# Kernel tuning notes

Measured on AMD Instinct MI355X. Metric: run time of the kernel, lower is better.

## Reference

```python
import jax, jax.numpy as jnp
import numpy as np

EMBED_DIM = 512

def setup_inputs() -> dict:
    key = jax.random.key(0)
    ks = jax.random.split(key, 5)
    D = EMBED_DIM
    x = jax.random.normal(ks[0], (4, 2048, D), dtype=jnp.float32)
    # qkv projection: weight [3D, D] (torch layout), bias [3D]
    qkv_w = jax.random.normal(ks[1], (3 * D, D), dtype=jnp.float32) * (D ** -0.5)
    qkv_b = jax.random.normal(ks[2], (3 * D,), dtype=jnp.float32) * 0.02
    out_w = jax.random.normal(ks[3], (D, D), dtype=jnp.float32) * (D ** -0.5)
    out_b = jax.random.normal(ks[4], (D,), dtype=jnp.float32) * 0.02
    return {"x": x, "qkv_w": qkv_w, "qkv_b": qkv_b, "out_w": out_w, "out_b": out_b}

def reference(x, qkv_w, qkv_b, out_w, out_b):
    D = x.shape[-1]
    scaling = D ** -0.5
    # qkv: [B, S, 3D]
    qkv = jnp.einsum('bsd,ed->bse', x, qkv_w) + qkv_b
    q, k, v = jnp.split(qkv, 3, axis=-1)
    q = q * scaling
    # scores: [B, S, S]
    attn = jnp.einsum('bqd,bkd->bqk', q, k)
    attn = jax.nn.softmax(attn, axis=-1)
    # dropout p=0.0 -> identity (eval-mode equivalent)
    out = jnp.einsum('bqk,bkd->bqd', attn, v)
    out = jnp.einsum('bsd,ed->bse', out, out_w) + out_b
    return out
```

## Files before the change

kernel.cpp:

```cpp
#include <hip/hip_runtime.h>

typedef _Float16 f16;
typedef _Float16 f16x2 __attribute__((ext_vector_type(2)));
typedef _Float16 f16x4 __attribute__((ext_vector_type(4)));
typedef _Float16 f16x8 __attribute__((ext_vector_type(8)));
typedef float f32x4 __attribute__((ext_vector_type(4)));
typedef float f32x16 __attribute__((ext_vector_type(16)));

#define MFMA16(a, b, c) __builtin_amdgcn_mfma_f32_16x16x32_f16((a), (b), (c), 0, 0, 0)
#define MFMA32(a, b, c) __builtin_amdgcn_mfma_f32_32x32x16_f16((a), (b), (c), 0, 0, 0)

typedef const __attribute__((address_space(1))) void gv_t;
typedef __attribute__((address_space(3))) void lv_t;

__global__ void cvt_all(const float* __restrict__ x, const float* __restrict__ qw,
                        const float* __restrict__ ow, f16* __restrict__ d) {
    int i = (blockIdx.x * 256 + threadIdx.x) * 4;
    const float* s;
    int off;
    if (i < 4194304) { s = x; off = i; }
    else if (i < 4980736) { s = qw; off = i - 4194304; }
    else { s = ow; off = i - 4980736; }
    float4 v = *(const float4*)(s + off);
    f16x4 o = {(f16)v.x, (f16)v.y, (f16)v.z, (f16)v.w};
    *(f16x4*)(d + i) = o;
}

template<int MODE>
__global__ __launch_bounds__(256, 3) void gemm_nt(const f16* __restrict__ A, const f16* __restrict__ W,
                                                  const float* __restrict__ bias, float* __restrict__ Cf,
                                                  f16* __restrict__ Qb, f16* __restrict__ Kb,
                                                  f16* __restrict__ Vt) {
    __shared__ f16 As[2][128 * 32];
    __shared__ f16 Bs[2][128 * 32];
    const int m0 = blockIdx.x * 128, n0 = blockIdx.y * 128;
    const int tid = threadIdx.x;
    const int w = tid >> 6, l = tid & 63;
    const int wm = w >> 1, wn = w & 1;
    const int lr = l & 15, lg = l >> 4;
    const int R = w * 16 + (l >> 2);
    const int ldsoff = w * 512;
    const int lidx = ldsoff + l * 8;
    const f16* ag = A + (size_t)(m0 + R) * 512 + (l & 3) * 8;
    const f16* bg = W + (size_t)(n0 + R) * 512 + (l & 3) * 8;
    (void)lidx;

#if __has_builtin(__builtin_amdgcn_global_load_lds)
#define GLDS(gp, lp) __builtin_amdgcn_global_load_lds((gv_t*)(gp), (lv_t*)(lp), 16, 0, 0)
#define STAGE(k0, buf) do {                                   \
        GLDS(ag + (k0), &As[buf][ldsoff]);                    \
        GLDS(ag + 64 * 512 + (k0), &As[buf][ldsoff + 2048]);  \
        GLDS(bg + (k0), &Bs[buf][ldsoff]);                    \
        GLDS(bg + 64 * 512 + (k0), &Bs[buf][ldsoff + 2048]);  \
    } while (0)
#else
#define STAGE(k0, buf) do {                                                      \
        *(f16x8*)&As[buf][lidx] = *(const f16x8*)(ag + (k0));                    \
        *(f16x8*)&As[buf][lidx + 2048] = *(const f16x8*)(ag + 64 * 512 + (k0));  \
        *(f16x8*)&Bs[buf][lidx] = *(const f16x8*)(bg + (k0));                    \
        *(f16x8*)&Bs[buf][lidx + 2048] = *(const f16x8*)(bg + 64 * 512 + (k0));  \
    } while (0)
#endif

    f32x4 acc[4][4] = {};
    STAGE(0, 0);
    __syncthreads();
    int cur = 0;
    for (int k0 = 0; k0 < 512; k0 += 32) {
        if (k0 + 32 < 512) STAGE(k0 + 32, cur ^ 1);
        f16x8 af[4], bf[4];
#pragma unroll
        for (int i = 0; i < 4; ++i) af[i] = *(f16x8*)&As[cur][(64 * wm + 16 * i + lr) * 32 + lg * 8];
#pragma unroll
        for (int i = 0; i < 4; ++i) bf[i] = *(f16x8*)&Bs[cur][(64 * wn + 16 * i + lr) * 32 + lg * 8];
        __builtin_amdgcn_s_setprio(1);
#pragma unroll
        for (int mf = 0; mf < 4; ++mf)
#pragma unroll
            for (int nf = 0; nf < 4; ++nf) acc[mf][nf] = MFMA16(af[mf], bf[nf], acc[mf][nf]);
        __builtin_amdgcn_s_setprio(0);
        __syncthreads();
        cur ^= 1;
    }
#pragma unroll
    for (int mf = 0; mf < 4; ++mf)
#pragma unroll
        for (int nf = 0; nf < 4; ++nf)
#pragma unroll
            for (int r = 0; r < 4; ++r) {
                int rr = 64 * wm + 16 * mf + 4 * lg + r;
                int cc = 64 * wn + 16 * nf + lr;
                int m = m0 + rr, e = n0 + cc;
                float val = acc[mf][nf][r] + bias[e];
                if (MODE == 0) {
                    int bb = m >> 11, s = m & 2047;
                    if (e < 512) {
                        Qb[((size_t)bb * 2048 + s) * 512 + e] = (f16)(val * 0.04419417382415922f);
                    } else if (e < 1024) {
                        int d = e - 512;
                        Kb[((((size_t)bb * 64 + (s >> 5)) * 32 + (d >> 4)) * 64
                            + ((d >> 3) & 1) * 32 + (s & 31)) * 8 + (d & 7)] = (f16)val;
                    } else {
                        int d = e - 1024;
                        Vt[((((size_t)bb * 16 + (d >> 5)) * 128 + (s >> 4)) * 64
                            + ((s >> 3) & 1) * 32 + (d & 31)) * 8 + (s & 7)] = (f16)val;
                    }
                } else {
                    Cf[(size_t)m * 512 + e] = val;
                }
            }
#undef STAGE
}

template<int NSPLIT, bool PART>
__global__ __launch_bounds__(512, 2) void flash_attn(const f16* __restrict__ Qb, const f16* __restrict__ Kb,
                                                     const f16* __restrict__ Vt, f16* __restrict__ AO,
                                                     f16* __restrict__ Opart, float* __restrict__ Ml) {
    __shared__ f16 Qs[32 * 512];
    __shared__ f16 P_lds[32 * 256];
    __shared__ float mbuf[32][8];
    __shared__ float lbuf[32][8];
    __shared__ float abuf[32];

    const int bid = blockIdx.x;
    const int xcd = bid & 7, slot = bid >> 3;
    const int b = xcd >> 1;
    const int t = slot * 2 + (xcd & 1);
    const int q0 = (t / NSPLIT) * 32;
    const int ks = t % NSPLIT;
    const int SPLITLEN = 2048 / NSPLIT;
    const int nkt = SPLITLEN / 256;

    const int tid = threadIdx.x;
    const int j = tid >> 6, l = tid & 63;
    const int q = l & 31, lh = l >> 5;

    const f16* Qg = Qb + ((size_t)b * 2048 + q0) * 512;
    const f16* Kg = Kb + ((size_t)b * 64 + (size_t)ks * (SPLITLEN / 32)) * 32 * 512;
    const f16* Vg = Vt + (size_t)b * 16 * 128 * 512 + (size_t)(ks * (SPLITLEN / 16)) * 512;

    for (int i = tid; i < 2048; i += 512) {
        int r = i >> 6, ch = i & 63;
        *(f16x8*)&Qs[r * 512 + ((ch ^ (r & 7)) * 8)] = *(const f16x8*)&Qg[(size_t)r * 512 + ch * 8];
    }

    f32x16 o[2] = {};
    float m_st = -1e30f, l_st = 0.f;
    char* Pq = (char*)&P_lds[0];
    const uint swz = ((uint)(q & 15)) << 4;
    const int qbase = q * 512, qx = q & 7;
    f16x8 kr[16], vr[8];
    {
        const f16* kp0 = Kg + (size_t)j * 32 * 512 + (size_t)l * 8;
#pragma unroll
        for (int i = 0; i < 16; ++i) kr[i] = *(const f16x8*)(kp0 + (size_t)i * 512);
    }
    __syncthreads();

    for (int kt = 0; kt < nkt; ++kt) {
        const int key0 = kt * 256;
        const f16* kp = Kg + ((size_t)((key0 >> 5) + j) * 32) * 512 + (size_t)l * 8;
        const f16* vpb = Vg + ((size_t)(2 * j) * 128 + (key0 >> 4)) * 512 + (size_t)l * 8;
#pragma unroll
        for (int i = 0; i < 4; ++i) {
            vr[2 * i] = *(const f16x8*)(vpb + (size_t)i * 512);
            vr[2 * i + 1] = *(const f16x8*)(vpb + (size_t)(128 + i) * 512);
        }
        f32x16 sA = {}, sB = {};
        __builtin_amdgcn_s_setprio(1);
#pragma unroll
        for (int kc = 0; kc < 32; kc += 2) {
            f16x8 k0 = kr[kc & 15];
            f16x8 k1 = kr[(kc & 15) + 1];
            if (kc < 16) {
                kr[kc] = *(const f16x8*)(kp + (size_t)(kc + 16) * 512);
                kr[kc + 1] = *(const f16x8*)(kp + (size_t)(kc + 17) * 512);
            }
            f16x8 q0f = *(f16x8*)&Qs[qbase + (((2 * kc + lh) ^ qx) * 8)];
            f16x8 q1f = *(f16x8*)&Qs[qbase + (((2 * kc + 2 + lh) ^ qx) * 8)];
            sA = MFMA32(k0, q0f, sA);
            sB = MFMA32(k1, q1f, sB);
        }
        __builtin_amdgcn_s_setprio(0);
        float s[16];
#pragma unroll
        for (int r = 0; r < 16; ++r) s[r] = sA[r] + sB[r];
        float mt = s[0];
#pragma unroll
        for (int r = 1; r < 16; ++r) mt = fmaxf(mt, s[r]);
        mt = fmaxf(mt, __shfl_xor(mt, 32));
        if (l < 32) mbuf[q][j] = mt;
        __syncthreads();
        float mnew = m_st;
        {
            float4 mv0 = *(float4*)&mbuf[q][0];
            float4 mv1 = *(float4*)&mbuf[q][4];
            mnew = fmaxf(mnew, fmaxf(fmaxf(mv0.x, mv0.y), fmaxf(mv0.z, mv0.w)));
            mnew = fmaxf(mnew, fmaxf(fmaxf(mv1.x, mv1.y), fmaxf(mv1.z, mv1.w)));
        }
        float alpha = __expf(m_st - mnew);
        if (l < 32) abuf[q] = alpha;
        float ps = 0.f;
#pragma unroll
        for (int r = 0; r < 16; ++r) {
            s[r] = __expf(s[r] - mnew);
            ps += s[r];
        }
        ps += __shfl_xor(ps, 32);
        if (l < 32) lbuf[q][j] = ps;
        {
            const uint rowb = (uint)q * 512;
#pragma unroll
            for (int i = 0; i < 4; ++i) {
                int key = 8 * i + 4 * lh + 32 * j;
                f16x4 pk = {(f16)s[4 * i], (f16)s[4 * i + 1], (f16)s[4 * i + 2], (f16)s[4 * i + 3]};
                *(f16x4*)(Pq + ((rowb + (uint)key * 2) ^ swz)) = pk;
            }
        }
        m_st = mnew;
        __syncthreads();
        if (kt + 1 < nkt) {
            const f16* kpn = Kg + ((size_t)(((key0 + 256) >> 5) + j) * 32) * 512 + (size_t)l * 8;
#pragma unroll
            for (int i = 0; i < 16; ++i) kr[i] = *(const f16x8*)(kpn + (size_t)i * 512);
        }
        {
            float4 lv0 = *(float4*)&lbuf[q][0];
            float4 lv1 = *(float4*)&lbuf[q][4];
            l_st = l_st * alpha + ((lv0.x + lv0.y) + (lv0.z + lv0.w))
                                + ((lv1.x + lv1.y) + (lv1.z + lv1.w));
        }
        float av[4][4];
#pragma unroll
        for (int g = 0; g < 4; ++g) {
            float4 a4 = *(float4*)&abuf[8 * g + 4 * lh];
            av[g][0] = a4.x; av[g][1] = a4.y; av[g][2] = a4.z; av[g][3] = a4.w;
        }
#pragma unroll
        for (int dt = 0; dt < 2; ++dt)
#pragma unroll
            for (int r = 0; r < 16; ++r) o[dt][r] *= av[r >> 2][r & 3];
        __builtin_amdgcn_s_setprio(1);
#pragma unroll
        for (int kk = 0; kk < 16; ++kk) {
            f16x8 v0 = vr[(kk & 3) * 2];
            f16x8 v1 = vr[(kk & 3) * 2 + 1];
            if (kk < 12) {
                vr[(kk & 3) * 2] = *(const f16x8*)(vpb + (size_t)(kk + 4) * 512);
                vr[(kk & 3) * 2 + 1] = *(const f16x8*)(vpb + (size_t)(128 + kk + 4) * 512);
            }
            f16x8 paf = *(f16x8*)(Pq + (((uint)q * 512 + (uint)(16 * kk + 8 * lh) * 2) ^ swz));
            o[0] = MFMA32(paf, v0, o[0]);
            o[1] = MFMA32(paf, v1, o[1]);
        }
        __builtin_amdgcn_s_setprio(0);
    }
    __syncthreads();
    if (l < 32) abuf[q] = l_st;
    if (PART && l < 32 && j == 0) {
        Ml[((size_t)bid * 32 + q) * 2 + 0] = m_st;
        Ml[((size_t)bid * 32 + q) * 2 + 1] = l_st;
    }
    __syncthreads();
    float iv[4][4];
#pragma unroll
    for (int g = 0; g < 4; ++g) {
        float4 a4 = *(float4*)&abuf[8 * g + 4 * lh];
        iv[g][0] = 1.f / a4.x; iv[g][1] = 1.f / a4.y; iv[g][2] = 1.f / a4.z; iv[g][3] = 1.f / a4.w;
    }
    f16* op = PART ? (Opart + (size_t)bid * 32 * 512 + 64 * j)
                   : (AO + ((size_t)(b * 2048 + q0)) * 512 + 64 * j);
#pragma unroll
    for (int r = 0; r < 16; ++r) {
        int qr = (r & 3) + 8 * (r >> 2) + 4 * lh;
        float inv = iv[r >> 2][r & 3];
#pragma unroll
        for (int dt = 0; dt < 2; ++dt)
            op[(size_t)qr * 512 + 32 * dt + q] = (f16)(o[dt][r] * inv);
    }
}

template<int NS>
__global__ __launch_bounds__(256) void combineN(const f16* __restrict__ Opart, const float* __restrict__ Ml,
                                                f16* __restrict__ AO) {
    int gid = blockIdx.x * 256 + threadIdx.x;
    int row = gid >> 6, col0 = (gid & 63) * 8;
    int b = row >> 11, qq = row & 2047;
    int qb = qq >> 5, qr = qq & 31;
    int bids[NS];
    float m[NS], ll[NS];
#pragma unroll
    for (int s = 0; s < NS; ++s) {
        int t = qb * NS + s;
        bids[s] = (t >> 1) * 8 + 2 * b + (t & 1);
        m[s] = Ml[((size_t)bids[s] * 32 + qr) * 2];
        ll[s] = Ml[((size_t)bids[s] * 32 + qr) * 2 + 1];
    }
    float M = m[0];
#pragma unroll
    for (int s = 1; s < NS; ++s) M = fmaxf(M, m[s]);
    float c[NS], W = 0.f;
#pragma unroll
    for (int s = 0; s < NS; ++s) {
        c[s] = __expf(m[s] - M) * ll[s];
        W += c[s];
    }
    float invW = 1.f / W;
    float av[8] = {};
#pragma unroll
    for (int s = 0; s < NS; ++s) {
        f16x8 v = *(const f16x8*)&Opart[((size_t)bids[s] * 32 + qr) * 512 + col0];
        float cs = c[s] * invW;
#pragma unroll
        for (int jj = 0; jj < 8; ++jj) av[jj] += cs * (float)v[jj];
    }
    f16x8 o8;
#pragma unroll
    for (int jj = 0; jj < 8; ++jj) o8[jj] = (f16)av[jj];
    *(f16x8*)&AO[(size_t)row * 512 + col0] = o8;
}

extern "C" void kernel_launch(void* const* d_in, const int* in_sizes, int n_in,
                              void* d_out, int out_size, void* d_ws, size_t ws_size,
                              hipStream_t stream) {
    (void)in_sizes; (void)n_in; (void)out_size;
    const float* x = (const float*)d_in[0];
    const float* qkv_w = (const float*)d_in[1];
    const float* qkv_b = (const float*)d_in[2];
    const float* out_w = (const float*)d_in[3];
    const float* out_b = (const float*)d_in[4];
    char* ws = (char*)d_ws;
    f16* xh    = (f16*)(ws + 0);
    f16* wqkvh = (f16*)(ws + 8388608);
    f16* wouth = (f16*)(ws + 9961472);
    f16* Qb    = (f16*)(ws + 10485760);
    f16* Kb    = (f16*)(ws + 18874368);
    f16* Vt    = (f16*)(ws + 27262976);
    f16* AO    = (f16*)(ws + 35651584);
    f16* Opart = (f16*)(ws + 44040192);
    float* Ml  = (float*)(ws + 44040192 + 16777216);
    const size_t NEED = 44040192ull + 16777216ull + 131072ull;
    (void)wqkvh; (void)wouth;

    cvt_all<<<5120, 256, 0, stream>>>(x, qkv_w, out_w, xh);

    gemm_nt<0><<<dim3(64, 12), 256, 0, stream>>>(xh, wqkvh, qkv_b, nullptr, Qb, Kb, Vt);

    if (ws_size >= NEED) {
        flash_attn<2, true><<<512, 512, 0, stream>>>(Qb, Kb, Vt, nullptr, Opart, Ml);
        combineN<2><<<2048, 256, 0, stream>>>(Opart, Ml, AO);
    } else {
        flash_attn<1, false><<<256, 512, 0, stream>>>(Qb, Kb, Vt, AO, nullptr, nullptr);
    }

    gemm_nt<1><<<dim3(64, 4), 256, 0, stream>>>(AO, wouth, out_b, (float*)d_out,
                                                nullptr, nullptr, nullptr);
}
```

Measured before the change: 118.0 us.

## Process 64 query rows per flash-attention block to reuse K/V tiles

Each attention block now handles 64 query rows instead of 32, so every K and V fragment loaded from global memory feeds two MFMAs, one per 32-row half. The grid is halved and the combine kernel and partial buffer indexing are updated for 64-row blocks. This is meant to halve K/V global traffic per query, at the cost of doubled LDS usage, more accumulator registers, and only 256 blocks, which may leave compute units underused.

```diff
diff --git a/kernel.cpp b/kernel.cpp
--- a/kernel.cpp
+++ b/kernel.cpp
@@ -116,17 +116,17 @@
 __global__ __launch_bounds__(512, 2) void flash_attn(const f16* __restrict__ Qb, const f16* __restrict__ Kb,
                                                      const f16* __restrict__ Vt, f16* __restrict__ AO,
                                                      f16* __restrict__ Opart, float* __restrict__ Ml) {
-    __shared__ f16 Qs[32 * 512];
-    __shared__ f16 P_lds[32 * 256];
-    __shared__ float mbuf[32][8];
-    __shared__ float lbuf[32][8];
-    __shared__ float abuf[32];
+    __shared__ f16 Qs[64 * 512];
+    __shared__ f16 P_lds[64 * 256];
+    __shared__ float mbuf[64][8];
+    __shared__ float lbuf[64][8];
+    __shared__ float abuf[64];
 
     const int bid = blockIdx.x;
     const int xcd = bid & 7, slot = bid >> 3;
     const int b = xcd >> 1;
     const int t = slot * 2 + (xcd & 1);
-    const int q0 = (t / NSPLIT) * 32;
+    const int q0 = (t / NSPLIT) * 64;
     const int ks = t % NSPLIT;
     const int SPLITLEN = 2048 / NSPLIT;
     const int nkt = SPLITLEN / 256;
@@ -139,21 +139,22 @@
     const f16* Kg = Kb + ((size_t)b * 64 + (size_t)ks * (SPLITLEN / 32)) * 32 * 512;
     const f16* Vg = Vt + (size_t)b * 16 * 128 * 512 + (size_t)(ks * (SPLITLEN / 16)) * 512;
 
-    for (int i = tid; i < 2048; i += 512) {
+    for (int i = tid; i < 4096; i += 512) {
         int r = i >> 6, ch = i & 63;
         *(f16x8*)&Qs[r * 512 + ((ch ^ (r & 7)) * 8)] = *(const f16x8*)&Qg[(size_t)r * 512 + ch * 8];
     }
 
-    f32x16 o[2] = {};
-    float m_st = -1e30f, l_st = 0.f;
+    f32x16 o[4] = {};
+    float m0_st = -1e30f, l0_st = 0.f;
+    float m1_st = -1e30f, l1_st = 0.f;
     char* Pq = (char*)&P_lds[0];
     const uint swz = ((uint)(q & 15)) << 4;
-    const int qbase = q * 512, qx = q & 7;
-    f16x8 kr[16], vr[8];
+    const int qb0 = q * 512, qb1 = (q + 32) * 512, qx = q & 7;
+    f16x8 kr[8], vr[8];
     {
         const f16* kp0 = Kg + (size_t)j * 32 * 512 + (size_t)l * 8;
 #pragma unroll
-        for (int i = 0; i < 16; ++i) kr[i] = *(const f16x8*)(kp0 + (size_t)i * 512);
+        for (int i = 0; i < 8; ++i) kr[i] = *(const f16x8*)(kp0 + (size_t)i * 512);
     }
     __syncthreads();
 
@@ -166,80 +167,98 @@
             vr[2 * i] = *(const f16x8*)(vpb + (size_t)i * 512);
             vr[2 * i + 1] = *(const f16x8*)(vpb + (size_t)(128 + i) * 512);
         }
-        f32x16 sA = {}, sB = {};
+        f32x16 sA0 = {}, sA1 = {};
         __builtin_amdgcn_s_setprio(1);
 #pragma unroll
-        for (int kc = 0; kc < 32; kc += 2) {
-            f16x8 k0 = kr[kc & 15];
-            f16x8 k1 = kr[(kc & 15) + 1];
-            if (kc < 16) {
-                kr[kc] = *(const f16x8*)(kp + (size_t)(kc + 16) * 512);
-                kr[kc + 1] = *(const f16x8*)(kp + (size_t)(kc + 17) * 512);
-            }
-            f16x8 q0f = *(f16x8*)&Qs[qbase + (((2 * kc + lh) ^ qx) * 8)];
-            f16x8 q1f = *(f16x8*)&Qs[qbase + (((2 * kc + 2 + lh) ^ qx) * 8)];
-            sA = MFMA32(k0, q0f, sA);
-            sB = MFMA32(k1, q1f, sB);
+        for (int kc = 0; kc < 32; ++kc) {
+            f16x8 kf = kr[kc & 7];
+            if (kc < 24) kr[kc & 7] = *(const f16x8*)(kp + (size_t)(kc + 8) * 512);
+            f16x8 qf0 = *(f16x8*)&Qs[qb0 + (((2 * kc + lh) ^ qx) * 8)];
+            f16x8 qf1 = *(f16x8*)&Qs[qb1 + (((2 * kc + lh) ^ qx) * 8)];
+            sA0 = MFMA32(kf, qf0, sA0);
+            sA1 = MFMA32(kf, qf1, sA1);
         }
         __builtin_amdgcn_s_setprio(0);
-        float s[16];
-#pragma unroll
-        for (int r = 0; r < 16; ++r) s[r] = sA[r] + sB[r];
-        float mt = s[0];
-#pragma unroll
-        for (int r = 1; r < 16; ++r) mt = fmaxf(mt, s[r]);
-        mt = fmaxf(mt, __shfl_xor(mt, 32));
-        if (l < 32) mbuf[q][j] = mt;
+        float s0[16], s1[16];
+#pragma unroll
+        for (int r = 0; r < 16; ++r) { s0[r] = sA0[r]; s1[r] = sA1[r]; }
+        float mt0 = s0[0], mt1 = s1[0];
+#pragma unroll
+        for (int r = 1; r < 16; ++r) { mt0 = fmaxf(mt0, s0[r]); mt1 = fmaxf(mt1, s1[r]); }
+        mt0 = fmaxf(mt0, __shfl_xor(mt0, 32));
+        mt1 = fmaxf(mt1, __shfl_xor(mt1, 32));
+        if (l < 32) { mbuf[q][j] = mt0; mbuf[q + 32][j] = mt1; }
         __syncthreads();
-        float mnew = m_st;
+        float mnew0 = m0_st, mnew1 = m1_st;
         {
-            float4 mv0 = *(float4*)&mbuf[q][0];
-            float4 mv1 = *(float4*)&mbuf[q][4];
-            mnew = fmaxf(mnew, fmaxf(fmaxf(mv0.x, mv0.y), fmaxf(mv0.z, mv0.w)));
-            mnew = fmaxf(mnew, fmaxf(fmaxf(mv1.x, mv1.y), fmaxf(mv1.z, mv1.w)));
-        }
-        float alpha = __expf(m_st - mnew);
-        if (l < 32) abuf[q] = alpha;
-        float ps = 0.f;
+            float4 a = *(float4*)&mbuf[q][0], c = *(float4*)&mbuf[q][4];
+            mnew0 = fmaxf(mnew0, fmaxf(fmaxf(a.x, a.y), fmaxf(a.z, a.w)));
+            mnew0 = fmaxf(mnew0, fmaxf(fmaxf(c.x, c.y), fmaxf(c.z, c.w)));
+            float4 d = *(float4*)&mbuf[q + 32][0], e = *(float4*)&mbuf[q + 32][4];
+            mnew1 = fmaxf(mnew1, fmaxf(fmaxf(d.x, d.y), fmaxf(d.z, d.w)));
+            mnew1 = fmaxf(mnew1, fmaxf(fmaxf(e.x, e.y), fmaxf(e.z, e.w)));
+        }
+        float alpha0 = __expf(m0_st - mnew0);
+        float alpha1 = __expf(m1_st - mnew1);
+        if (l < 32) { abuf[q] = alpha0; abuf[q + 32] = alpha1; }
+        float ps0 = 0.f, ps1 = 0.f;
 #pragma unroll
         for (int r = 0; r < 16; ++r) {
-            s[r] = __expf(s[r] - mnew);
-            ps += s[r];
-        }
-        ps += __shfl_xor(ps, 32);
-        if (l < 32) lbuf[q][j] = ps;
+            s0[r] = __expf(s0[r] - mnew0);
+            ps0 += s0[r];
+            s1[r] = __expf(s1[r] - mnew1);
+            ps1 += s1[r];
+        }
+        ps0 += __shfl_xor(ps0, 32);
+        ps1 += __shfl_xor(ps1, 32);
+        if (l < 32) { lbuf[q][j] = ps0; lbuf[q + 32][j] = ps1; }
         {
-            const uint rowb = (uint)q * 512;
+            const uint rowb0 = (uint)q * 512;
+            const uint rowb1 = (uint)(q + 32) * 512;
 #pragma unroll
             for (int i = 0; i < 4; ++i) {
                 int key = 8 * i + 4 * lh + 32 * j;
-                f16x4 pk = {(f16)s[4 * i], (f16)s[4 * i + 1], (f16)s[4 * i + 2], (f16)s[4 * i + 3]};
-                *(f16x4*)(Pq + ((rowb + (uint)key * 2) ^ swz)) = pk;
+                f16x4 pk0 = {(f16)s0[4 * i], (f16)s0[4 * i + 1], (f16)s0[4 * i + 2], (f16)s0[4 * i + 3]};
+                f16x4 pk1 = {(f16)s1[4 * i], (f16)s1[4 * i + 1], (f16)s1[4 * i + 2], (f16)s1[4 * i + 3]};
+                *(f16x4*)(Pq + ((rowb0 + (uint)key * 2) ^ swz)) = pk0;
+                *(f16x4*)(Pq + ((rowb1 + (uint)key * 2) ^ swz)) = pk1;
             }
         }
-        m_st = mnew;
+        m0_st = mnew0;
+        m1_st = mnew1;
         __syncthreads();
         if (kt + 1 < nkt) {
             const f16* kpn = Kg + ((size_t)(((key0 + 256) >> 5) + j) * 32) * 512 + (size_t)l * 8;
 #pragma unroll
-            for (int i = 0; i < 16; ++i) kr[i] = *(const f16x8*)(kpn + (size_t)i * 512);
+            for (int i = 0; i < 8; ++i) kr[i] = *(const f16x8*)(kpn + (size_t)i * 512);
         }
         {
             float4 lv0 = *(float4*)&lbuf[q][0];
             float4 lv1 = *(float4*)&lbuf[q][4];
-            l_st = l_st * alpha + ((lv0.x + lv0.y) + (lv0.z + lv0.w))
-                                + ((lv1.x + lv1.y) + (lv1.z + lv1.w));
-        }
-        float av[4][4];
-#pragma unroll
-        for (int g = 0; g < 4; ++g) {
-            float4 a4 = *(float4*)&abuf[8 * g + 4 * lh];
-            av[g][0] = a4.x; av[g][1] = a4.y; av[g][2] = a4.z; av[g][3] = a4.w;
-        }
-#pragma unroll
-        for (int dt = 0; dt < 2; ++dt)
-#pragma unroll
-            for (int r = 0; r < 16; ++r) o[dt][r] *= av[r >> 2][r & 3];
+            l0_st = l0_st * alpha0 + ((lv0.x + lv0.y) + (lv0.z + lv0.w))
+                                   + ((lv1.x + lv1.y) + (lv1.z + lv1.w));
+            float4 lw0 = *(float4*)&lbuf[q + 32][0];
+            float4 lw1 = *(float4*)&lbuf[q + 32][4];
+            l1_st = l1_st * alpha1 + ((lw0.x + lw0.y) + (lw0.z + lw0.w))
+                                   + ((lw1.x + lw1.y) + (lw1.z + lw1.w));
+        }
+        {
+            float av0[4][4], av1[4][4];
+#pragma unroll
+            for (int g = 0; g < 4; ++g) {
+                float4 a4 = *(float4*)&abuf[8 * g + 4 * lh];
+                av0[g][0] = a4.x; av0[g][1] = a4.y; av0[g][2] = a4.z; av0[g][3] = a4.w;
+                float4 b4 = *(float4*)&abuf[32 + 8 * g + 4 * lh];
+                av1[g][0] = b4.x; av1[g][1] = b4.y; av1[g][2] = b4.z; av1[g][3] = b4.w;
+            }
+#pragma unroll
+            for (int dt = 0; dt < 2; ++dt)
+#pragma unroll
+                for (int r = 0; r < 16; ++r) {
+                    o[dt][r] *= av0[r >> 2][r & 3];
+                    o[2 + dt][r] *= av1[r >> 2][r & 3];
+                }
+        }
         __builtin_amdgcn_s_setprio(1);
 #pragma unroll
         for (int kk = 0; kk < 16; ++kk) {
@@ -249,34 +268,44 @@
                 vr[(kk & 3) * 2] = *(const f16x8*)(vpb + (size_t)(kk + 4) * 512);
                 vr[(kk & 3) * 2 + 1] = *(const f16x8*)(vpb + (size_t)(128 + kk + 4) * 512);
             }
-            f16x8 paf = *(f16x8*)(Pq + (((uint)q * 512 + (uint)(16 * kk + 8 * lh) * 2) ^ swz));
-            o[0] = MFMA32(paf, v0, o[0]);
-            o[1] = MFMA32(paf, v1, o[1]);
+            f16x8 paf0 = *(f16x8*)(Pq + (((uint)q * 512 + (uint)(16 * kk + 8 * lh) * 2) ^ swz));
+            f16x8 paf1 = *(f16x8*)(Pq + (((uint)(q + 32) * 512 + (uint)(16 * kk + 8 * lh) * 2) ^ swz));
+            o[0] = MFMA32(paf0, v0, o[0]);
+            o[1] = MFMA32(paf0, v1, o[1]);
+            o[2] = MFMA32(paf1, v0, o[2]);
+            o[3] = MFMA32(paf1, v1, o[3]);
         }
         __builtin_amdgcn_s_setprio(0);
     }
     __syncthreads();
-    if (l < 32) abuf[q] = l_st;
+    if (l < 32) { abuf[q] = l0_st; abuf[q + 32] = l1_st; }
     if (PART && l < 32 && j == 0) {
-        Ml[((size_t)bid * 32 + q) * 2 + 0] = m_st;
-        Ml[((size_t)bid * 32 + q) * 2 + 1] = l_st;
+        Ml[((size_t)bid * 64 + q) * 2 + 0] = m0_st;
+        Ml[((size_t)bid * 64 + q) * 2 + 1] = l0_st;
+        Ml[((size_t)bid * 64 + q + 32) * 2 + 0] = m1_st;
+        Ml[((size_t)bid * 64 + q + 32) * 2 + 1] = l1_st;
     }
     __syncthreads();
-    float iv[4][4];
+    float iv0[4][4], iv1[4][4];
 #pragma unroll
     for (int g = 0; g < 4; ++g) {
         float4 a4 = *(float4*)&abuf[8 * g + 4 * lh];
-        iv[g][0] = 1.f / a4.x; iv[g][1] = 1.f / a4.y; iv[g][2] = 1.f / a4.z; iv[g][3] = 1.f / a4.w;
-    }
-    f16* op = PART ? (Opart + (size_t)bid * 32 * 512 + 64 * j)
+        iv0[g][0] = 1.f / a4.x; iv0[g][1] = 1.f / a4.y; iv0[g][2] = 1.f / a4.z; iv0[g][3] = 1.f / a4.w;
+        float4 b4 = *(float4*)&abuf[32 + 8 * g + 4 * lh];
+        iv1[g][0] = 1.f / b4.x; iv1[g][1] = 1.f / b4.y; iv1[g][2] = 1.f / b4.z; iv1[g][3] = 1.f / b4.w;
+    }
+    f16* op = PART ? (Opart + (size_t)bid * 64 * 512 + 64 * j)
                    : (AO + ((size_t)(b * 2048 + q0)) * 512 + 64 * j);
 #pragma unroll
     for (int r = 0; r < 16; ++r) {
         int qr = (r & 3) + 8 * (r >> 2) + 4 * lh;
-        float inv = iv[r >> 2][r & 3];
-#pragma unroll
-        for (int dt = 0; dt < 2; ++dt)
-            op[(size_t)qr * 512 + 32 * dt + q] = (f16)(o[dt][r] * inv);
+        float i0 = iv0[r >> 2][r & 3];
+        float i1 = iv1[r >> 2][r & 3];
+#pragma unroll
+        for (int dt = 0; dt < 2; ++dt) {
+            op[(size_t)qr * 512 + 32 * dt + q] = (f16)(o[dt][r] * i0);
+            op[(size_t)(qr + 32) * 512 + 32 * dt + q] = (f16)(o[2 + dt][r] * i1);
+        }
     }
 }
 
@@ -286,15 +315,15 @@
     int gid = blockIdx.x * 256 + threadIdx.x;
     int row = gid >> 6, col0 = (gid & 63) * 8;
     int b = row >> 11, qq = row & 2047;
-    int qb = qq >> 5, qr = qq & 31;
+    int qb = qq >> 6, qr = qq & 63;
     int bids[NS];
     float m[NS], ll[NS];
 #pragma unroll
     for (int s = 0; s < NS; ++s) {
         int t = qb * NS + s;
         bids[s] = (t >> 1) * 8 + 2 * b + (t & 1);
-        m[s] = Ml[((size_t)bids[s] * 32 + qr) * 2];
-        ll[s] = Ml[((size_t)bids[s] * 32 + qr) * 2 + 1];
+        m[s] = Ml[((size_t)bids[s] * 64 + qr) * 2];
+        ll[s] = Ml[((size_t)bids[s] * 64 + qr) * 2 + 1];
     }
     float M = m[0];
 #pragma unroll
@@ -309,7 +338,7 @@
     float av[8] = {};
 #pragma unroll
     for (int s = 0; s < NS; ++s) {
-        f16x8 v = *(const f16x8*)&Opart[((size_t)bids[s] * 32 + qr) * 512 + col0];
+        f16x8 v = *(const f16x8*)&Opart[((size_t)bids[s] * 64 + qr) * 512 + col0];
         float cs = c[s] * invW;
 #pragma unroll
         for (int jj = 0; jj < 8; ++jj) av[jj] += cs * (float)v[jj];
@@ -340,17 +369,16 @@
     f16* Opart = (f16*)(ws + 44040192);
     float* Ml  = (float*)(ws + 44040192 + 16777216);
     const size_t NEED = 44040192ull + 16777216ull + 131072ull;
-    (void)wqkvh; (void)wouth;
 
     cvt_all<<<5120, 256, 0, stream>>>(x, qkv_w, out_w, xh);
 
     gemm_nt<0><<<dim3(64, 12), 256, 0, stream>>>(xh, wqkvh, qkv_b, nullptr, Qb, Kb, Vt);
 
     if (ws_size >= NEED) {
-        flash_attn<2, true><<<512, 512, 0, stream>>>(Qb, Kb, Vt, nullptr, Opart, Ml);
+        flash_attn<2, true><<<256, 512, 0, stream>>>(Qb, Kb, Vt, nullptr, Opart, Ml);
         combineN<2><<<2048, 256, 0, stream>>>(Opart, Ml, AO);
     } else {
-        flash_attn<1, false><<<256, 512, 0, stream>>>(Qb, Kb, Vt, AO, nullptr, nullptr);
+        flash_attn<1, false><<<128, 512, 0, stream>>>(Qb, Kb, Vt, AO, nullptr, nullptr);
     }
 
     gemm_nt<1><<<dim3(64, 4), 256, 0, stream>>>(AO, wouth, out_b, (float*)d_out,
```

New measurement: 133.4 us. 1.13x slower.
